# Kernel optimization log

Measured on AMD Instinct MI355X. Metric: run time of the kernel, lower is better.

The kernel has to match this reference:

```python
import jax, jax.numpy as jnp
import numpy as np

B, N, C, H, M, CC = 8, 1024, 1280, 20, 77, 768
FF = 4 * C
AQ_BITS = 8
W_BITS = 8


def fq_sym(x, bits=AQ_BITS):
    # per-tensor symmetric fake quant with straight-through estimator
    qmax = 2.0 ** (bits - 1) - 1.0
    delta = jnp.maximum(jnp.max(jnp.abs(x)), 1e-8) / qmax
    q = jnp.clip(jnp.round(x / delta), -qmax - 1.0, qmax) * delta
    return x + jax.lax.stop_gradient(q - x)


def fq_zero(x, bits=W_BITS):
    # asymmetric, always_zero (zero point = 0): for softmax probs in [0,1]
    levels = 2.0 ** bits - 1.0
    delta = jnp.maximum(jnp.max(x), 1e-8) / levels
    q = jnp.clip(jnp.round(x / delta), 0.0, levels) * delta
    return x + jax.lax.stop_gradient(q - x)


def layer_norm(x, g, b, eps=1e-5):
    mu = jnp.mean(x, axis=-1, keepdims=True)
    var = jnp.var(x, axis=-1, keepdims=True)
    return (x - mu) * jax.lax.rsqrt(var + eps) * g + b


def attention(x, ctx, Wq, Wk, Wv, Wo, bo, heads):
    b, n, c = x.shape
    m = ctx.shape[1]
    dh = c // heads
    q = fq_sym(x @ Wq)
    k = fq_sym(ctx @ Wk)
    v = fq_sym(ctx @ Wv)
    q = q.reshape(b, n, heads, dh).transpose(0, 2, 1, 3)
    k = k.reshape(b, m, heads, dh).transpose(0, 2, 1, 3)
    v = v.reshape(b, m, heads, dh).transpose(0, 2, 1, 3)
    scores = jnp.einsum('bhnd,bhmd->bhnm', q, k) * (dh ** -0.5)
    w = jax.nn.softmax(scores, axis=-1)
    w = fq_zero(w)  # quantized softmax weights (forces explicit prob materialization)
    out = jnp.einsum('bhnm,bhmd->bhnd', w, v)
    out = out.transpose(0, 2, 1, 3).reshape(b, n, c)
    return out @ Wo + bo


def geglu_ff(x, W1, b1, W2, b2):
    h = x @ W1 + b1
    a, g = jnp.split(h, 2, axis=-1)
    return (a * jax.nn.gelu(g)) @ W2 + b2


def setup_inputs() -> dict:
    key = jax.random.key(0)
    ks = jax.random.split(key, 16)
    s = 0.02
    return {
        'x': jax.random.normal(ks[0], (B, N, C), jnp.float32),
        'ctx': jax.random.normal(ks[1], (B, M, CC), jnp.float32),
        'ln1_g': jnp.ones((C,), jnp.float32), 'ln1_b': jnp.zeros((C,), jnp.float32),
        'ln2_g': jnp.ones((C,), jnp.float32), 'ln2_b': jnp.zeros((C,), jnp.float32),
        'ln3_g': jnp.ones((C,), jnp.float32), 'ln3_b': jnp.zeros((C,), jnp.float32),
        'Wq1': jax.random.normal(ks[2], (C, C), jnp.float32) * s,
        'Wk1': jax.random.normal(ks[3], (C, C), jnp.float32) * s,
        'Wv1': jax.random.normal(ks[4], (C, C), jnp.float32) * s,
        'Wo1': jax.random.normal(ks[5], (C, C), jnp.float32) * s,
        'bo1': jnp.zeros((C,), jnp.float32),
        'Wq2': jax.random.normal(ks[6], (C, C), jnp.float32) * s,
        'Wk2': jax.random.normal(ks[7], (CC, C), jnp.float32) * s,
        'Wv2': jax.random.normal(ks[8], (CC, C), jnp.float32) * s,
        'Wo2': jax.random.normal(ks[9], (C, C), jnp.float32) * s,
        'bo2': jnp.zeros((C,), jnp.float32),
        'Wff1': jax.random.normal(ks[10], (C, 2 * FF), jnp.float32) * s,
        'bff1': jnp.zeros((2 * FF,), jnp.float32),
        'Wff2': jax.random.normal(ks[11], (FF, C), jnp.float32) * s,
        'bff2': jnp.zeros((C,), jnp.float32),
        'heads': H,
    }


def reference(x, ctx, ln1_g, ln1_b, ln2_g, ln2_b, ln3_g, ln3_b,
              Wq1, Wk1, Wv1, Wo1, bo1, Wq2, Wk2, Wv2, Wo2, bo2,
              Wff1, bff1, Wff2, bff2, heads):
    h = attention(layer_norm(x, ln1_g, ln1_b), layer_norm(x, ln1_g, ln1_b),
                  Wq1, Wk1, Wv1, Wo1, bo1, heads)
    x = x + h
    h = attention(layer_norm(x, ln2_g, ln2_b), ctx, Wq2, Wk2, Wv2, Wo2, bo2, heads)
    x = x + h
    x = x + geglu_ff(layer_norm(x, ln3_g, ln3_b), Wff1, bff1, Wff2, bff2)
    return x
```

## Files before the change

kernel.cpp:

```cpp
#include <hip/hip_runtime.h>

typedef __attribute__((ext_vector_type(8))) short bf16x8;
typedef __attribute__((ext_vector_type(4))) float f32x4;

#define DEV __device__ __forceinline__
#define MF(A, B, CACC) CACC = __builtin_amdgcn_mfma_f32_16x16x32_bf16(A, B, CACC, 0, 0, 0)

DEV ushort f2b(float f) {
  unsigned u = __float_as_uint(f);
  u += 0x7fffu + ((u >> 16) & 1u);
  return (ushort)(u >> 16);
}
DEV float b2f(ushort u) { return __uint_as_float(((unsigned)u) << 16); }

DEV void gl_lds16(ushort* lds_base, const ushort* gp) {
  __builtin_amdgcn_global_load_lds(
      (__attribute__((address_space(1))) const void*)gp,
      (__attribute__((address_space(3))) void*)lds_base, 16, 0, 0);
}

__global__ void k_zero(unsigned* p, int n) {
  int i = blockIdx.x * blockDim.x + threadIdx.x;
  if (i < n) p[i] = 0u;
}

__global__ __launch_bounds__(256) void k_wt(const float* __restrict__ W,
                                            ushort* __restrict__ WT, int K, int N) {
  __shared__ float T[32][33];
  int k0 = blockIdx.y * 32, n0 = blockIdx.x * 32;
  int tx = threadIdx.x & 31, ty = threadIdx.x >> 5;
  #pragma unroll
  for (int r = ty; r < 32; r += 8) {
    int k = k0 + r, n = n0 + tx;
    T[r][tx] = (k < K && n < N) ? W[(size_t)k * N + n] : 0.f;
  }
  __syncthreads();
  #pragma unroll
  for (int r = ty; r < 32; r += 8) {
    int n = n0 + r, k = k0 + tx;
    if (n < N && k < K) WT[(size_t)n * K + k] = f2b(T[tx][r]);
  }
}

__global__ void k_cvt(const float* __restrict__ in, ushort* __restrict__ out, int n) {
  int i = blockIdx.x * 256 + threadIdx.x;
  if (i < n) out[i] = f2b(in[i]);
}

__global__ __launch_bounds__(256) void k_ln(const float* __restrict__ x,
    const float* __restrict__ g, const float* __restrict__ b,
    ushort* __restrict__ out) {
  const int C = 1280;
  int row = blockIdx.x, tid = threadIdx.x;
  const float* xr = x + (size_t)row * C;
  float v0 = xr[tid], v1 = xr[tid + 256], v2 = xr[tid + 512],
        v3 = xr[tid + 768], v4 = xr[tid + 1024];
  float s = v0 + v1 + v2 + v3 + v4;
  float ss = v0 * v0 + v1 * v1 + v2 * v2 + v3 * v3 + v4 * v4;
  #pragma unroll
  for (int off = 32; off; off >>= 1) {
    s += __shfl_down(s, off);
    ss += __shfl_down(ss, off);
  }
  __shared__ float red[8];
  __shared__ float mu_s, rstd_s;
  int wave = tid >> 6, lane = tid & 63;
  if (lane == 0) { red[wave] = s; red[4 + wave] = ss; }
  __syncthreads();
  if (tid == 0) {
    float S = red[0] + red[1] + red[2] + red[3];
    float SS = red[4] + red[5] + red[6] + red[7];
    float mu = S / C;
    float var = SS / C - mu * mu;
    mu_s = mu;
    rstd_s = rsqrtf(var + 1e-5f);
  }
  __syncthreads();
  float mu = mu_s, rstd = rstd_s;
  size_t o = (size_t)row * C + tid;
  out[o]        = f2b((v0 - mu) * rstd * g[tid]        + b[tid]);
  out[o + 256]  = f2b((v1 - mu) * rstd * g[tid + 256]  + b[tid + 256]);
  out[o + 512]  = f2b((v2 - mu) * rstd * g[tid + 512]  + b[tid + 512]);
  out[o + 768]  = f2b((v3 - mu) * rstd * g[tid + 768]  + b[tid + 768]);
  out[o + 1024] = f2b((v4 - mu) * rstd * g[tid + 1024] + b[tid + 1024]);
}

DEV void st1(float v, int r_, int c_, int ldc, const float* resid,
             float* Cf, ushort* Cb) {
  size_t o = (size_t)r_ * ldc + c_;
  if (resid) v += resid[o];
  if (Cf) Cf[o] = v;
  if (Cb) Cb[o] = f2b(v);
}
DEV float epi4(f32x4 v, int rbase, int c_, int M, int N, int ldc,
               const float* bias, const float* resid, float* Cf, ushort* Cb) {
  float v0 = v.x, v1 = v.y, v2 = v.z, v3 = v.w;
  float am = fmaxf(fmaxf(fabsf(v0), fabsf(v1)), fmaxf(fabsf(v2), fabsf(v3)));
  if (c_ < N) {
    float bb = bias ? bias[c_] : 0.f;
    v0 += bb; v1 += bb; v2 += bb; v3 += bb;
    if (rbase + 0 < M) st1(v0, rbase + 0, c_, ldc, resid, Cf, Cb);
    if (rbase + 1 < M) st1(v1, rbase + 1, c_, ldc, resid, Cf, Cb);
    if (rbase + 2 < M) st1(v2, rbase + 2, c_, ldc, resid, Cf, Cb);
    if (rbase + 3 < M) st1(v3, rbase + 3, c_, ldc, resid, Cf, Cb);
  }
  return am;
}

__global__ __launch_bounds__(256) void k_gemm(
    const ushort* __restrict__ A, int lda,
    const ushort* __restrict__ BT, int ldb,
    float* __restrict__ Cf, ushort* __restrict__ Cb, int ldc,
    const float* __restrict__ bias, const float* __restrict__ resid,
    unsigned* am_slot, int M, int N, int K, int slcN) {
  __shared__ __align__(16) ushort SAB[8192];
  int tid = threadIdx.x;
  int wave = tid >> 6, lane = tid & 63;
  int q = lane >> 4, mi = lane & 15;
  int wr = (wave >> 1) * 64, wc = (wave & 1) * 64;
  int bm0 = blockIdx.y * 128, bn0 = blockIdx.x * 128;
  f32x4 c00 = {}, c01 = {}, c02 = {}, c03 = {};
  f32x4 c10 = {}, c11 = {}, c12 = {}, c13 = {};
  f32x4 c20 = {}, c21 = {}, c22 = {}, c23 = {};
  f32x4 c30 = {}, c31 = {}, c32 = {}, c33 = {};
  for (int k0 = 0; k0 < K; k0 += 32) {
    __syncthreads();
    #pragma unroll
    for (int t = 0; t < 4; t++) {
      int c = wave * 256 + t * 64 + lane;
      const ushort* gp;
      if (c < 512) {
        int r = c >> 2, kc = (c & 3) << 3;
        int gr = bm0 + r; if (gr >= M) gr = M - 1;
        gp = A + (size_t)gr * lda + k0 + kc;
      } else {
        int c2 = c - 512;
        int r = c2 >> 2, kc = (c2 & 3) << 3;
        int gn = bn0 + r; if (gn >= N) gn = N - 1;
        gp = BT + (size_t)gn * ldb + k0 + kc;
      }
      gl_lds16(&SAB[(wave * 256 + t * 64) * 8], gp);
    }
    __syncthreads();
    const ushort* Ab = &SAB[(wr + mi) * 32 + q * 8];
    const ushort* Bb = &SAB[4096 + (wc + mi) * 32 + q * 8];
    bf16x8 a0 = *(const bf16x8*)(Ab);
    bf16x8 a1 = *(const bf16x8*)(Ab + 512);
    bf16x8 a2 = *(const bf16x8*)(Ab + 1024);
    bf16x8 a3 = *(const bf16x8*)(Ab + 1536);
    bf16x8 b0 = *(const bf16x8*)(Bb);
    bf16x8 b1 = *(const bf16x8*)(Bb + 512);
    bf16x8 b2 = *(const bf16x8*)(Bb + 1024);
    bf16x8 b3 = *(const bf16x8*)(Bb + 1536);
    MF(a0, b0, c00); MF(a0, b1, c01); MF(a0, b2, c02); MF(a0, b3, c03);
    MF(a1, b0, c10); MF(a1, b1, c11); MF(a1, b2, c12); MF(a1, b3, c13);
    MF(a2, b0, c20); MF(a2, b1, c21); MF(a2, b2, c22); MF(a2, b3, c23);
    MF(a3, b0, c30); MF(a3, b1, c31); MF(a3, b2, c32); MF(a3, b3, c33);
  }
  int rb = bm0 + wr + q * 4, cb = bn0 + wc + mi;
  float am = 0.f;
  am = fmaxf(am, epi4(c00, rb +  0, cb +  0, M, N, ldc, bias, resid, Cf, Cb));
  am = fmaxf(am, epi4(c01, rb +  0, cb + 16, M, N, ldc, bias, resid, Cf, Cb));
  am = fmaxf(am, epi4(c02, rb +  0, cb + 32, M, N, ldc, bias, resid, Cf, Cb));
  am = fmaxf(am, epi4(c03, rb +  0, cb + 48, M, N, ldc, bias, resid, Cf, Cb));
  am = fmaxf(am, epi4(c10, rb + 16, cb +  0, M, N, ldc, bias, resid, Cf, Cb));
  am = fmaxf(am, epi4(c11, rb + 16, cb + 16, M, N, ldc, bias, resid, Cf, Cb));
  am = fmaxf(am, epi4(c12, rb + 16, cb + 32, M, N, ldc, bias, resid, Cf, Cb));
  am = fmaxf(am, epi4(c13, rb + 16, cb + 48, M, N, ldc, bias, resid, Cf, Cb));
  am = fmaxf(am, epi4(c20, rb + 32, cb +  0, M, N, ldc, bias, resid, Cf, Cb));
  am = fmaxf(am, epi4(c21, rb + 32, cb + 16, M, N, ldc, bias, resid, Cf, Cb));
  am = fmaxf(am, epi4(c22, rb + 32, cb + 32, M, N, ldc, bias, resid, Cf, Cb));
  am = fmaxf(am, epi4(c23, rb + 32, cb + 48, M, N, ldc, bias, resid, Cf, Cb));
  am = fmaxf(am, epi4(c30, rb + 48, cb +  0, M, N, ldc, bias, resid, Cf, Cb));
  am = fmaxf(am, epi4(c31, rb + 48, cb + 16, M, N, ldc, bias, resid, Cf, Cb));
  am = fmaxf(am, epi4(c32, rb + 48, cb + 32, M, N, ldc, bias, resid, Cf, Cb));
  am = fmaxf(am, epi4(c33, rb + 48, cb + 48, M, N, ldc, bias, resid, Cf, Cb));
  if (am_slot) {
    #pragma unroll
    for (int off = 32; off; off >>= 1) am = fmaxf(am, __shfl_down(am, off));
    if (lane == 0) atomicMax(am_slot + bn0 / slcN, __float_as_uint(am));
  }
}

__global__ void k_quant8(const ushort* __restrict__ in, ushort* __restrict__ out,
                         const unsigned* __restrict__ slotb, int n8,
                         int colw8, int ld, int slcw) {
  int i = blockIdx.x * 256 + threadIdx.x;
  if (i >= n8) return;
  int row = i / colw8, c8 = i - row * colw8;
  int col = c8 * 8;
  size_t a = (size_t)row * ld + col;
  float delta = fmaxf(__uint_as_float(slotb[col / slcw]), 1e-8f) * (1.f / 127.f);
  bf16x8 v = *(const bf16x8*)(in + a);
  bf16x8 r;
  #pragma unroll
  for (int j = 0; j < 8; j++) {
    float x = b2f((ushort)v[j]);
    float y = fminf(fmaxf(rintf(x / delta), -128.f), 127.f) * delta;
    r[j] = (short)f2b(y);
  }
  *(bf16x8*)(out + a) = r;
}

__global__ __launch_bounds__(256) void k_vt(const ushort* __restrict__ vq,
    ushort* __restrict__ vT, int H, int Mr, int Mpad, int ldv) {
  __shared__ __align__(16) ushort T[64][72];
  int bh = blockIdx.y, b = bh / H, h = bh % H;
  int m0 = blockIdx.x * 64;
  int tid = threadIdx.x;
  #pragma unroll
  for (int c = tid; c < 512; c += 256) {
    int mm = c >> 3, dc = (c & 7) << 3;
    int m = m0 + mm;
    int4 val = make_int4(0, 0, 0, 0);
    if (m < Mr) val = *(const int4*)(vq + ((size_t)b * Mr + m) * ldv + h * 64 + dc);
    *(int4*)&T[mm][dc] = val;
  }
  __syncthreads();
  #pragma unroll
  for (int c = tid; c < 512; c += 256) {
    int dd = c >> 3, mc = (c & 7) << 3;
    unsigned w0 = (unsigned)T[mc + 0][dd] | ((unsigned)T[mc + 1][dd] << 16);
    unsigned w1 = (unsigned)T[mc + 2][dd] | ((unsigned)T[mc + 3][dd] << 16);
    unsigned w2 = (unsigned)T[mc + 4][dd] | ((unsigned)T[mc + 5][dd] << 16);
    unsigned w3 = (unsigned)T[mc + 6][dd] | ((unsigned)T[mc + 7][dd] << 16);
    int4 val = make_int4((int)w0, (int)w1, (int)w2, (int)w3);
    *(int4*)(vT + ((size_t)bh * 64 + dd) * Mpad + m0 + mc) = val;
  }
}

#define NEGI -3.0e38f
#define ONLUPD(SA, SB, SC, SD, MRUN, ZRUN) do { \
  float e0  = b0_  ? (SA).x * cs : NEGI; \
  float e1  = b1_  ? (SA).y * cs : NEGI; \
  float e2  = b2_  ? (SA).z * cs : NEGI; \
  float e3  = b3_  ? (SA).w * cs : NEGI; \
  float e4  = b4_  ? (SB).x * cs : NEGI; \
  float e5  = b5_  ? (SB).y * cs : NEGI; \
  float e6  = b6_  ? (SB).z * cs : NEGI; \
  float e7  = b7_  ? (SB).w * cs : NEGI; \
  float e8  = b8_  ? (SC).x * cs : NEGI; \
  float e9  = b9_  ? (SC).y * cs : NEGI; \
  float e10 = b10_ ? (SC).z * cs : NEGI; \
  float e11 = b11_ ? (SC).w * cs : NEGI; \
  float e12 = b12_ ? (SD).x * cs : NEGI; \
  float e13 = b13_ ? (SD).y * cs : NEGI; \
  float e14 = b14_ ? (SD).z * cs : NEGI; \
  float e15 = b15_ ? (SD).w * cs : NEGI; \
  float tm = fmaxf(fmaxf(fmaxf(fmaxf(e0, e1), fmaxf(e2, e3)), \
                         fmaxf(fmaxf(e4, e5), fmaxf(e6, e7))), \
                   fmaxf(fmaxf(fmaxf(e8, e9), fmaxf(e10, e11)), \
                         fmaxf(fmaxf(e12, e13), fmaxf(e14, e15)))); \
  float mn = fmaxf(MRUN, tm); \
  float zs = exp2f(e0 - mn)  + exp2f(e1 - mn)  + exp2f(e2 - mn)  + exp2f(e3 - mn) \
           + exp2f(e4 - mn)  + exp2f(e5 - mn)  + exp2f(e6 - mn)  + exp2f(e7 - mn) \
           + exp2f(e8 - mn)  + exp2f(e9 - mn)  + exp2f(e10 - mn) + exp2f(e11 - mn) \
           + exp2f(e12 - mn) + exp2f(e13 - mn) + exp2f(e14 - mn) + exp2f(e15 - mn); \
  ZRUN = ZRUN * exp2f(MRUN - mn) + zs; MRUN = mn; \
} while (0)

__global__ __launch_bounds__(256) void k_attn1(
    const ushort* __restrict__ qq, const ushort* __restrict__ kq,
    float2* __restrict__ rs, unsigned* __restrict__ pmax,
    int H, int N, int Mr, int ldq, int ldk, float cs) {
  __shared__ __align__(16) ushort Qs[128][72];
  __shared__ __align__(16) ushort Ks[64][72];
  int tid = threadIdx.x;
  int wave = tid >> 6, lane = tid & 63;
  int q = lane >> 4, mi = lane & 15;
  int bh = blockIdx.y, b = bh / H, h = bh % H;
  int r0 = blockIdx.x * 128;
  #pragma unroll
  for (int c = tid; c < 1024; c += 256) {
    int r = c >> 3, dc = (c & 7) << 3;
    *(int4*)&Qs[r][dc] = *(const int4*)(qq + ((size_t)b * N + r0 + r) * ldq + h * 64 + dc);
  }
  float m0r = NEGI, z0r = 0.f, m1r = NEGI, z1r = 0.f;
  int nt = (Mr + 63) >> 6;
  for (int mt = 0; mt < nt; mt++) {
    __syncthreads();
    #pragma unroll
    for (int c = tid; c < 512; c += 256) {
      int mm = c >> 3, dc = (c & 7) << 3;
      int m = mt * 64 + mm;
      int4 val = make_int4(0, 0, 0, 0);
      if (m < Mr) val = *(const int4*)(kq + ((size_t)b * Mr + m) * ldk + h * 64 + dc);
      *(int4*)&Ks[mm][dc] = val;
    }
    __syncthreads();
    f32x4 s0 = {}, s1 = {}, s2 = {}, s3 = {};
    f32x4 s4 = {}, s5 = {}, s6 = {}, s7 = {};
    #pragma unroll
    for (int kc = 0; kc < 2; kc++) {
      bf16x8 qv0 = *(const bf16x8*)&Qs[wave * 32 + mi][kc * 32 + q * 8];
      bf16x8 qv1 = *(const bf16x8*)&Qs[wave * 32 + 16 + mi][kc * 32 + q * 8];
      bf16x8 k0v = *(const bf16x8*)&Ks[mi][kc * 32 + q * 8];
      bf16x8 k1v = *(const bf16x8*)&Ks[16 + mi][kc * 32 + q * 8];
      bf16x8 k2v = *(const bf16x8*)&Ks[32 + mi][kc * 32 + q * 8];
      bf16x8 k3v = *(const bf16x8*)&Ks[48 + mi][kc * 32 + q * 8];
      MF(k0v, qv0, s0); MF(k1v, qv0, s1); MF(k2v, qv0, s2); MF(k3v, qv0, s3);
      MF(k0v, qv1, s4); MF(k1v, qv1, s5); MF(k2v, qv1, s6); MF(k3v, qv1, s7);
    }
    int kb = mt * 64 + q * 4;
    bool b0_  = kb + 0  < Mr, b1_  = kb + 1  < Mr, b2_  = kb + 2  < Mr, b3_  = kb + 3  < Mr;
    bool b4_  = kb + 16 < Mr, b5_  = kb + 17 < Mr, b6_  = kb + 18 < Mr, b7_  = kb + 19 < Mr;
    bool b8_  = kb + 32 < Mr, b9_  = kb + 33 < Mr, b10_ = kb + 34 < Mr, b11_ = kb + 35 < Mr;
    bool b12_ = kb + 48 < Mr, b13_ = kb + 49 < Mr, b14_ = kb + 50 < Mr, b15_ = kb + 51 < Mr;
    ONLUPD(s0, s1, s2, s3, m0r, z0r);
    ONLUPD(s4, s5, s6, s7, m1r, z1r);
  }
  float mo0 = fmaxf(m0r, __shfl_xor(m0r, 16));
  mo0 = fmaxf(mo0, __shfl_xor(mo0, 32));
  float zz0 = z0r * exp2f(m0r - mo0);
  zz0 += __shfl_xor(zz0, 16);
  zz0 += __shfl_xor(zz0, 32);
  float mo1 = fmaxf(m1r, __shfl_xor(m1r, 16));
  mo1 = fmaxf(mo1, __shfl_xor(mo1, 32));
  float zz1 = z1r * exp2f(m1r - mo1);
  zz1 += __shfl_xor(zz1, 16);
  zz1 += __shfl_xor(zz1, 32);
  if (q == 0) {
    float2 st; st.x = mo0; st.y = zz0;
    rs[(size_t)bh * N + r0 + wave * 32 + mi] = st;
    st.x = mo1; st.y = zz1;
    rs[(size_t)bh * N + r0 + wave * 32 + 16 + mi] = st;
  }
  float pm = fmaxf(1.f / zz0, 1.f / zz1);
  #pragma unroll
  for (int off = 32; off; off >>= 1) pm = fmaxf(pm, __shfl_down(pm, off));
  if (lane == 0) atomicMax(pmax, __float_as_uint(pm));
}

DEV ushort q8lvl(float s, float cs, float mc) {
  float p = fminf(rintf(exp2f(fmaf(s, cs, -mc))), 255.f);
  return (ushort)(__float_as_uint(p) >> 16);
}

#define PWR(RB, SA, SB, SC, SD, M0_, M1_, M2_, M3_) do { \
  Ps[(RB) + 0][mi]      = ok0 ? q8lvl((SA).x, cs, M0_) : (ushort)0; \
  Ps[(RB) + 1][mi]      = ok0 ? q8lvl((SA).y, cs, M1_) : (ushort)0; \
  Ps[(RB) + 2][mi]      = ok0 ? q8lvl((SA).z, cs, M2_) : (ushort)0; \
  Ps[(RB) + 3][mi]      = ok0 ? q8lvl((SA).w, cs, M3_) : (ushort)0; \
  Ps[(RB) + 0][16 + mi] = ok1 ? q8lvl((SB).x, cs, M0_) : (ushort)0; \
  Ps[(RB) + 1][16 + mi] = ok1 ? q8lvl((SB).y, cs, M1_) : (ushort)0; \
  Ps[(RB) + 2][16 + mi] = ok1 ? q8lvl((SB).z, cs, M2_) : (ushort)0; \
  Ps[(RB) + 3][16 + mi] = ok1 ? q8lvl((SB).w, cs, M3_) : (ushort)0; \
  Ps[(RB) + 0][32 + mi] = ok2 ? q8lvl((SC).x, cs, M0_) : (ushort)0; \
  Ps[(RB) + 1][32 + mi] = ok2 ? q8lvl((SC).y, cs, M1_) : (ushort)0; \
  Ps[(RB) + 2][32 + mi] = ok2 ? q8lvl((SC).z, cs, M2_) : (ushort)0; \
  Ps[(RB) + 3][32 + mi] = ok2 ? q8lvl((SC).w, cs, M3_) : (ushort)0; \
  Ps[(RB) + 0][48 + mi] = ok3 ? q8lvl((SD).x, cs, M0_) : (ushort)0; \
  Ps[(RB) + 1][48 + mi] = ok3 ? q8lvl((SD).y, cs, M1_) : (ushort)0; \
  Ps[(RB) + 2][48 + mi] = ok3 ? q8lvl((SD).z, cs, M2_) : (ushort)0; \
  Ps[(RB) + 3][48 + mi] = ok3 ? q8lvl((SD).w, cs, M3_) : (ushort)0; \
} while (0)

#define OSTORE(RRBASE, OA, OB, OC, OD) do { \
  size_t base = ((size_t)b * N + (RRBASE)) * C + h * 64 + mi; \
  ao[base]              = f2b((OA).x * delta); ao[base + C]          = f2b((OA).y * delta); \
  ao[base + 2 * C]      = f2b((OA).z * delta); ao[base + 3 * C]      = f2b((OA).w * delta); \
  ao[base + 16]         = f2b((OB).x * delta); ao[base + C + 16]     = f2b((OB).y * delta); \
  ao[base + 2 * C + 16] = f2b((OB).z * delta); ao[base + 3 * C + 16] = f2b((OB).w * delta); \
  ao[base + 32]         = f2b((OC).x * delta); ao[base + C + 32]     = f2b((OC).y * delta); \
  ao[base + 2 * C + 32] = f2b((OC).z * delta); ao[base + 3 * C + 32] = f2b((OC).w * delta); \
  ao[base + 48]         = f2b((OD).x * delta); ao[base + C + 48]     = f2b((OD).y * delta); \
  ao[base + 2 * C + 48] = f2b((OD).z * delta); ao[base + 3 * C + 48] = f2b((OD).w * delta); \
} while (0)

__global__ __launch_bounds__(256) void k_attn2(
    const ushort* __restrict__ qq, const ushort* __restrict__ kq,
    const ushort* __restrict__ vT, const float2* __restrict__ rs,
    const unsigned* __restrict__ pmax, ushort* __restrict__ ao,
    int H, int N, int Mr, int Mpad, int ldq, int ldk, float cs) {
  const int C = 1280;
  __shared__ __align__(16) ushort Qs[128][72];
  __shared__ __align__(16) ushort Ks[64][72];
  __shared__ __align__(16) ushort Vs[64][72];
  __shared__ __align__(16) ushort Ps[128][72];
  int tid = threadIdx.x;
  int wave = tid >> 6, lane = tid & 63;
  int q = lane >> 4, mi = lane & 15;
  int bh = blockIdx.y, b = bh / H, h = bh % H;
  int r0 = blockIdx.x * 128;
  #pragma unroll
  for (int c = tid; c < 1024; c += 256) {
    int r = c >> 3, dc = (c & 7) << 3;
    *(int4*)&Qs[r][dc] = *(const int4*)(qq + ((size_t)b * N + r0 + r) * ldq + h * 64 + dc);
  }
  int rb0 = wave * 32 + q * 4, rb1 = rb0 + 16;
  float delta = fmaxf(__uint_as_float(*pmax), 1e-8f) * (1.f / 255.f);
  float ldl = __log2f(delta);
  float2 u0 = rs[(size_t)bh * N + r0 + rb0 + 0];
  float2 u1 = rs[(size_t)bh * N + r0 + rb0 + 1];
  float2 u2 = rs[(size_t)bh * N + r0 + rb0 + 2];
  float2 u3 = rs[(size_t)bh * N + r0 + rb0 + 3];
  float2 u4 = rs[(size_t)bh * N + r0 + rb1 + 0];
  float2 u5 = rs[(size_t)bh * N + r0 + rb1 + 1];
  float2 u6 = rs[(size_t)bh * N + r0 + rb1 + 2];
  float2 u7 = rs[(size_t)bh * N + r0 + rb1 + 3];
  float mc0 = u0.x + __log2f(u0.y) + ldl;
  float mc1 = u1.x + __log2f(u1.y) + ldl;
  float mc2 = u2.x + __log2f(u2.y) + ldl;
  float mc3 = u3.x + __log2f(u3.y) + ldl;
  float mc4 = u4.x + __log2f(u4.y) + ldl;
  float mc5 = u5.x + __log2f(u5.y) + ldl;
  float mc6 = u6.x + __log2f(u6.y) + ldl;
  float mc7 = u7.x + __log2f(u7.y) + ldl;
  f32x4 o0 = {}, o1 = {}, o2 = {}, o3 = {};
  f32x4 o4 = {}, o5 = {}, o6 = {}, o7 = {};
  int nt = (Mr + 63) >> 6;
  for (int mt = 0; mt < nt; mt++) {
    __syncthreads();
    #pragma unroll
    for (int c = tid; c < 512; c += 256) {
      int mm = c >> 3, dc = (c & 7) << 3;
      int m = mt * 64 + mm;
      int4 val = make_int4(0, 0, 0, 0);
      if (m < Mr) val = *(const int4*)(kq + ((size_t)b * Mr + m) * ldk + h * 64 + dc);
      *(int4*)&Ks[mm][dc] = val;
      *(int4*)&Vs[mm][dc] = *(const int4*)(vT + ((size_t)bh * 64 + mm) * Mpad + mt * 64 + dc);
    }
    __syncthreads();
    f32x4 s0 = {}, s1 = {}, s2 = {}, s3 = {};
    f32x4 s4 = {}, s5 = {}, s6 = {}, s7 = {};
    #pragma unroll
    for (int kc = 0; kc < 2; kc++) {
      bf16x8 aq0 = *(const bf16x8*)&Qs[wave * 32 + mi][kc * 32 + q * 8];
      bf16x8 aq1 = *(const bf16x8*)&Qs[wave * 32 + 16 + mi][kc * 32 + q * 8];
      bf16x8 k0v = *(const bf16x8*)&Ks[mi][kc * 32 + q * 8];
      bf16x8 k1v = *(const bf16x8*)&Ks[16 + mi][kc * 32 + q * 8];
      bf16x8 k2v = *(const bf16x8*)&Ks[32 + mi][kc * 32 + q * 8];
      bf16x8 k3v = *(const bf16x8*)&Ks[48 + mi][kc * 32 + q * 8];
      MF(aq0, k0v, s0); MF(aq0, k1v, s1); MF(aq0, k2v, s2); MF(aq0, k3v, s3);
      MF(aq1, k0v, s4); MF(aq1, k1v, s5); MF(aq1, k2v, s6); MF(aq1, k3v, s7);
    }
    int mlim = Mr - mt * 64;
    bool ok0 = (mi      < mlim);
    bool ok1 = (16 + mi < mlim);
    bool ok2 = (32 + mi < mlim);
    bool ok3 = (48 + mi < mlim);
    PWR(rb0, s0, s1, s2, s3, mc0, mc1, mc2, mc3);
    PWR(rb1, s4, s5, s6, s7, mc4, mc5, mc6, mc7);
    asm volatile("s_waitcnt lgkmcnt(0)" ::: "memory");
    __builtin_amdgcn_sched_barrier(0);
    #pragma unroll
    for (int kc = 0; kc < 2; kc++) {
      bf16x8 ap0 = *(const bf16x8*)&Ps[wave * 32 + mi][kc * 32 + q * 8];
      bf16x8 ap1 = *(const bf16x8*)&Ps[wave * 32 + 16 + mi][kc * 32 + q * 8];
      bf16x8 v0 = *(const bf16x8*)&Vs[mi][kc * 32 + q * 8];
      bf16x8 v1 = *(const bf16x8*)&Vs[16 + mi][kc * 32 + q * 8];
      bf16x8 v2 = *(const bf16x8*)&Vs[32 + mi][kc * 32 + q * 8];
      bf16x8 v3 = *(const bf16x8*)&Vs[48 + mi][kc * 32 + q * 8];
      MF(ap0, v0, o0); MF(ap0, v1, o1); MF(ap0, v2, o2); MF(ap0, v3, o3);
      MF(ap1, v0, o4); MF(ap1, v1, o5); MF(ap1, v2, o6); MF(ap1, v3, o7);
    }
  }
  int rr0 = r0 + wave * 32 + q * 4;
  OSTORE(rr0, o0, o1, o2, o3);
  OSTORE(rr0 + 16, o4, o5, o6, o7);
}

#define BAR __builtin_amdgcn_s_barrier()
#define LGKM0 do { asm volatile("s_waitcnt lgkmcnt(0)" ::: "memory"); \
                   __builtin_amdgcn_sched_barrier(0); } while (0)
#define VM6 asm volatile("s_waitcnt vmcnt(6)" ::: "memory")
#define VM0 asm volatile("s_waitcnt vmcnt(0)" ::: "memory")
#define PRIO1 __builtin_amdgcn_s_setprio(1)
#define PRIO0 __builtin_amdgcn_s_setprio(0)

#define RDA01(P) do { \
  fa00 = *(const bf16x8*)&(P)[c0];        fa01 = *(const bf16x8*)&(P)[c1]; \
  fa10 = *(const bf16x8*)&(P)[1024 + c0]; fa11 = *(const bf16x8*)&(P)[1024 + c1]; } while (0)
#define RDA23(P) do { \
  fa20 = *(const bf16x8*)&(P)[2048 + c0]; fa21 = *(const bf16x8*)&(P)[2048 + c1]; \
  fa30 = *(const bf16x8*)&(P)[3072 + c0]; fa31 = *(const bf16x8*)&(P)[3072 + c1]; } while (0)
#define RDB(P, H) do { \
  b00 = *(const bf16x8*)&(P)[(H) + c0];        b01 = *(const bf16x8*)&(P)[(H) + c1]; \
  b10 = *(const bf16x8*)&(P)[(H) + 1024 + c0]; b11 = *(const bf16x8*)&(P)[(H) + 1024 + c1]; \
  b20 = *(const bf16x8*)&(P)[(H) + 2048 + c0]; b21 = *(const bf16x8*)&(P)[(H) + 2048 + c1]; \
  b30 = *(const bf16x8*)&(P)[(H) + 3072 + c0]; b31 = *(const bf16x8*)&(P)[(H) + 3072 + c1]; } while (0)
#define RDB8(P) RDB(P, 0)

#define MM8(AX0, AX1, AY0, AY1, C0, C1, C2, C3, D0, D1, D2, D3) \
  MF(AX0, b00, C0); MF(AX1, b01, C0); MF(AX0, b10, C1); MF(AX1, b11, C1); \
  MF(AX0, b20, C2); MF(AX1, b21, C2); MF(AX0, b30, C3); MF(AX1, b31, C3); \
  MF(AY0, b00, D0); MF(AY1, b01, D0); MF(AY0, b10, D1); MF(AY1, b11, D1); \
  MF(AY0, b20, D2); MF(AY1, b21, D2); MF(AY0, b30, D3); MF(AY1, b31, D3)

#define GB8(AP, BP, DB, KT) \
  RDA01(AP); RDB8(BP); \
  stB(DB, KT, 0); stB(DB, KT, 1); stA(DB, KT, 0); \
  BAR; LGKM0; \
  PRIO1; MM8(fa00, fa01, fa10, fa11, c00, c01, c02, c03, c10, c11, c12, c13); PRIO0; \
  BAR; \
  RDA23(AP); \
  stA(DB, KT, 1); stA(DB, KT, 2); stA(DB, KT, 3); \
  BAR; LGKM0; \
  PRIO1; MM8(fa20, fa21, fa30, fa31, c20, c21, c22, c23, c30, c31, c32, c33); PRIO0; \
  VM6; BAR;

#define GT8(AP, BP) \
  RDA01(AP); RDB8(BP); \
  BAR; LGKM0; \
  PRIO1; MM8(fa00, fa01, fa10, fa11, c00, c01, c02, c03, c10, c11, c12, c13); PRIO0; \
  BAR; \
  RDA23(AP); \
  BAR; LGKM0; \
  PRIO1; MM8(fa20, fa21, fa30, fa31, c20, c21, c22, c23, c30, c31, c32, c33); PRIO0;

__global__ __launch_bounds__(512) void k_gemm8(
    const ushort* __restrict__ A, int lda,
    const ushort* __restrict__ BT, int ldb,
    float* __restrict__ Cf, ushort* __restrict__ Cb, int ldc,
    const float* __restrict__ bias, const float* __restrict__ resid,
    unsigned* am_slot, int M, int N, int K, int slcN) {
  __shared__ __align__(16) ushort SAB[73728];
  int tid = threadIdx.x;
  int wave = tid >> 6, lane = tid & 63;
  int q = lane >> 4, mi = lane & 15;
  int wm = wave >> 1, wn = wave & 1;
  int lr = lane >> 3;
  int lc = ((lane & 7) ^ lr) * 8;

  int NBN = N >> 7;
  int nblk = (M >> 8) * NBN;
  int cpx = nblk >> 3;
  int wg = blockIdx.x;
  int swz = (wg & 7) * cpx + (wg >> 3);
  int bm0 = (swz / NBN) << 8, bn0 = (swz % NBN) << 7;

  const int swzr = (mi & 7) * 8;
  int c0 = (q * 8) ^ swzr, c1 = (32 + q * 8) ^ swzr;
  const ushort* A0p = &SAB[(wm * 64 + mi) * 64];
  const ushort* B0p = &SAB[16384 + (wn * 64 + mi) * 64];
  const ushort* A1p = A0p + 24576; const ushort* B1p = B0p + 24576;
  const ushort* A2p = A0p + 49152; const ushort* B2p = B0p + 49152;

  const ushort* gA = A  + (size_t)(bm0 + wave * 8 + lr) * lda + lc;
  const ushort* gB = BT + (size_t)(bn0 + wave * 8 + lr) * ldb + lc;
  ushort* lA = &SAB[wave * 512];
  ushort* lB = &SAB[16384 + wave * 512];

  auto stA = [&](int bb, int kt, int call) {
    gl_lds16(lA + bb * 24576 + call * 4096,
             gA + (size_t)call * 64 * lda + (size_t)kt * 64);
  };
  auto stB = [&](int bb, int kt, int call) {
    gl_lds16(lB + bb * 24576 + call * 4096,
             gB + (size_t)call * 64 * ldb + (size_t)kt * 64);
  };

  f32x4 c00 = {}, c01 = {}, c02 = {}, c03 = {};
  f32x4 c10 = {}, c11 = {}, c12 = {}, c13 = {};
  f32x4 c20 = {}, c21 = {}, c22 = {}, c23 = {};
  f32x4 c30 = {}, c31 = {}, c32 = {}, c33 = {};
  bf16x8 fa00, fa01, fa10, fa11, fa20, fa21, fa30, fa31;
  bf16x8 b00, b01, b10, b11, b20, b21, b30, b31;

  stB(0, 0, 0); stB(0, 0, 1);
  stA(0, 0, 0); stA(0, 0, 1); stA(0, 0, 2); stA(0, 0, 3);
  stB(1, 1, 0); stB(1, 1, 1);
  stA(1, 1, 0); stA(1, 1, 1); stA(1, 1, 2); stA(1, 1, 3);
  VM6; BAR;

  int NT = K >> 6, NTm = NT - 2;
  for (int t = 0; t < NTm; t += 3) {
    GB8(A0p, B0p, 2, t + 2);
    GB8(A1p, B1p, 0, t + 3);
    GB8(A2p, B2p, 1, t + 4);
  }
  GT8(A0p, B0p);
  VM0; BAR;
  GT8(A1p, B1p);

  int rb = bm0 + wm * 64 + q * 4, cb = bn0 + wn * 64 + mi;
  float am = 0.f;
  am = fmaxf(am, epi4(c00, rb +  0, cb +  0, M, N, ldc, bias, resid, Cf, Cb));
  am = fmaxf(am, epi4(c01, rb +  0, cb + 16, M, N, ldc, bias, resid, Cf, Cb));
  am = fmaxf(am, epi4(c02, rb +  0, cb + 32, M, N, ldc, bias, resid, Cf, Cb));
  am = fmaxf(am, epi4(c03, rb +  0, cb + 48, M, N, ldc, bias, resid, Cf, Cb));
  am = fmaxf(am, epi4(c10, rb + 16, cb +  0, M, N, ldc, bias, resid, Cf, Cb));
  am = fmaxf(am, epi4(c11, rb + 16, cb + 16, M, N, ldc, bias, resid, Cf, Cb));
  am = fmaxf(am, epi4(c12, rb + 16, cb + 32, M, N, ldc, bias, resid, Cf, Cb));
  am = fmaxf(am, epi4(c13, rb + 16, cb + 48, M, N, ldc, bias, resid, Cf, Cb));
  am = fmaxf(am, epi4(c20, rb + 32, cb +  0, M, N, ldc, bias, resid, Cf, Cb));
  am = fmaxf(am, epi4(c21, rb + 32, cb + 16, M, N, ldc, bias, resid, Cf, Cb));
  am = fmaxf(am, epi4(c22, rb + 32, cb + 32, M, N, ldc, bias, resid, Cf, Cb));
  am = fmaxf(am, epi4(c23, rb + 32, cb + 48, M, N, ldc, bias, resid, Cf, Cb));
  am = fmaxf(am, epi4(c30, rb + 48, cb +  0, M, N, ldc, bias, resid, Cf, Cb));
  am = fmaxf(am, epi4(c31, rb + 48, cb + 16, M, N, ldc, bias, resid, Cf, Cb));
  am = fmaxf(am, epi4(c32, rb + 48, cb + 32, M, N, ldc, bias, resid, Cf, Cb));
  am = fmaxf(am, epi4(c33, rb + 48, cb + 48, M, N, ldc, bias, resid, Cf, Cb));
  if (am_slot) {
    #pragma unroll
    for (int off = 32; off; off >>= 1) am = fmaxf(am, __shfl_down(am, off));
    if (lane == 0) atomicMax(am_slot + bn0 / slcN, __float_as_uint(am));
  }
}

DEV ushort ggel(float a, float g) {
  float u = 1.5957691216057308f * g * (1.f + 0.044715f * g * g);
  float s = 1.f / (1.f + __expf(-u));
  return f2b(a * g * s);
}
DEV void epi4g(f32x4 va, f32x4 vg, size_t base, float ba, float bg,
               ushort* __restrict__ GG) {
  GG[base]         = ggel(va.x + ba, vg.x + bg);
  GG[base + 5120]  = ggel(va.y + ba, vg.y + bg);
  GG[base + 10240] = ggel(va.z + ba, vg.z + bg);
  GG[base + 15360] = ggel(va.w + ba, vg.w + bg);
}
#define EPIN(nn, P0, Q0, P1, Q1, P2, Q2, P3, Q3) do { \
  int cg = colBase + nn * 16 + mi; \
  float ba = bias[cg], bg = bias[5120 + cg]; \
  size_t b0_ = (size_t)rowBase * 5120 + cg; \
  epi4g(P0, Q0, b0_,             ba, bg, GG); \
  epi4g(P1, Q1, b0_ + 16 * 5120, ba, bg, GG); \
  epi4g(P2, Q2, b0_ + 32 * 5120, ba, bg, GG); \
  epi4g(P3, Q3, b0_ + 48 * 5120, ba, bg, GG); \
} while (0)

__global__ __launch_bounds__(512) void k_ff1_8p(
    const ushort* __restrict__ A,
    const ushort* __restrict__ BT,
    const float* __restrict__ bias,
    ushort* __restrict__ GG) {
  __shared__ __align__(16) ushort SAB[65536];
  int tid = threadIdx.x;
  int wave = tid >> 6, lane = tid & 63;
  int q = lane >> 4, mi = lane & 15;
  int wm = wave >> 1, wn = wave & 1;
  int lr = lane >> 3;
  int lc = ((lane & 7) ^ lr) * 8;

  int wg = blockIdx.x;
  int swz = (wg & 7) * 160 + (wg >> 3);
  int bm0 = (swz & 31) * 256, bn0 = (swz >> 5) * 128;

  const int swzr = (mi & 7) * 8;
  int c0 = (q * 8) ^ swzr, c1 = (32 + q * 8) ^ swzr;
  const ushort* A0p = &SAB[(wm * 64 + mi) * 64];
  const ushort* B0p = &SAB[16384 + (wn * 64 + mi) * 64];
  const ushort* A1p = A0p + 32768;
  const ushort* B1p = B0p + 32768;

  const ushort* gA  = A  + (size_t)(bm0 + wave * 8 + lr) * 1280 + lc;
  const ushort* gBa = BT + (size_t)(bn0 + wave * 8 + lr) * 1280 + lc;
  const ushort* gBg = BT + (size_t)(5120 + bn0 + wave * 8 + lr) * 1280 + lc;
  ushort* lA = &SAB[wave * 512];
  ushort* lB = &SAB[16384 + wave * 512];

  auto stA = [&](int bb, int kt, int call) {
    gl_lds16(lA + bb * 32768 + call * 4096,
             gA + (size_t)call * 81920 + (size_t)kt * 64);
  };
  auto stBa = [&](int bb, int kt, int call) {
    gl_lds16(lB + bb * 32768 + call * 4096,
             gBa + (size_t)call * 81920 + (size_t)kt * 64);
  };
  auto stBg = [&](int bb, int kt, int call) {
    gl_lds16(lB + bb * 32768 + (call + 2) * 4096,
             gBg + (size_t)call * 81920 + (size_t)kt * 64);
  };

  f32x4 cA00 = {}, cA01 = {}, cA02 = {}, cA03 = {};
  f32x4 cA10 = {}, cA11 = {}, cA12 = {}, cA13 = {};
  f32x4 cA20 = {}, cA21 = {}, cA22 = {}, cA23 = {};
  f32x4 cA30 = {}, cA31 = {}, cA32 = {}, cA33 = {};
  f32x4 cG00 = {}, cG01 = {}, cG02 = {}, cG03 = {};
  f32x4 cG10 = {}, cG11 = {}, cG12 = {}, cG13 = {};
  f32x4 cG20 = {}, cG21 = {}, cG22 = {}, cG23 = {};
  f32x4 cG30 = {}, cG31 = {}, cG32 = {}, cG33 = {};
  bf16x8 fa00, fa01, fa10, fa11, fa20, fa21, fa30, fa31;
  bf16x8 b00, b01, b10, b11, b20, b21, b30, b31;

  stBa(0, 0, 0); stBa(0, 0, 1); stBg(0, 0, 0); stBg(0, 0, 1);
  stA(0, 0, 0); stA(0, 0, 1); stA(0, 0, 2); stA(0, 0, 3);
  stBa(1, 1, 0); stBa(1, 1, 1);
  stA(1, 1, 0); stA(1, 1, 1); stA(1, 1, 2); stA(1, 1, 3);
  VM6; BAR;

  for (int it = 0; it < 10; ++it) {
    int t1 = 2 * it + 1;
    int s0 = t1 + 1; if (s0 > 19) s0 = 19;
    int s1 = t1 + 2; if (s1 > 19) s1 = 19;
    RDA01(A0p); RDB(B0p, 0);
    stBg(1, t1, 0); stBg(1, t1, 1);
    BAR; LGKM0;
    PRIO1; MM8(fa00, fa01, fa10, fa11, cA00, cA01, cA02, cA03,
               cA10, cA11, cA12, cA13); PRIO0;
    BAR;
    RDA23(A0p);
    stBa(0, s0, 0); stBa(0, s0, 1);
    BAR; LGKM0;
    PRIO1; MM8(fa20, fa21, fa30, fa31, cA20, cA21, cA22, cA23,
               cA30, cA31, cA32, cA33); PRIO0;
    BAR;
    RDB(B0p, 8192);
    stA(0, s0, 0); stA(0, s0, 1);
    BAR; LGKM0;
    PRIO1; MM8(fa00, fa01, fa10, fa11, cG00, cG01, cG02, cG03,
               cG10, cG11, cG12, cG13); PRIO0;
    BAR;
    stA(0, s0, 2); stA(0, s0, 3);
    BAR;
    PRIO1; MM8(fa20, fa21, fa30, fa31, cG20, cG21, cG22, cG23,
               cG30, cG31, cG32, cG33); PRIO0;
    VM6; BAR;
    RDA01(A1p); RDB(B1p, 0);
    stBg(0, s0, 0); stBg(0, s0, 1);
    BAR; LGKM0;
    PRIO1; MM8(fa00, fa01, fa10, fa11, cA00, cA01, cA02, cA03,
               cA10, cA11, cA12, cA13); PRIO0;
    BAR;
    RDA23(A1p);
    stBa(1, s1, 0); stBa(1, s1, 1);
    BAR; LGKM0;
    PRIO1; MM8(fa20, fa21, fa30, fa31, cA20, cA21, cA22, cA23,
               cA30, cA31, cA32, cA33); PRIO0;
    BAR;
    RDB(B1p, 8192);
    stA(1, s1, 0); stA(1, s1, 1);
    BAR; LGKM0;
    PRIO1; MM8(fa00, fa01, fa10, fa11, cG00, cG01, cG02, cG03,
               cG10, cG11, cG12, cG13); PRIO0;
    BAR;
    stA(1, s1, 2); stA(1, s1, 3);
    BAR;
    PRIO1; MM8(fa20, fa21, fa30, fa31, cG20, cG21, cG22, cG23,
               cG30, cG31, cG32, cG33); PRIO0;
    VM6; BAR;
  }

  int colBase = bn0 + wn * 64;
  int rowBase = bm0 + wm * 64 + q * 4;
  EPIN(0, cA00, cG00, cA10, cG10, cA20, cG20, cA30, cG30);
  EPIN(1, cA01, cG01, cA11, cG11, cA21, cG21, cA31, cG31);
  EPIN(2, cA02, cG02, cA12, cG12, cA22, cG22, cA32, cG32);
  EPIN(3, cA03, cG03, cA13, cG13, cA23, cG23, cA33, cG33);
}

extern "C" void kernel_launch(void* const* d_in, const int* in_sizes, int n_in,
                              void* d_out, int out_size, void* d_ws, size_t ws_size,
                              hipStream_t stream) {
  const float* x_in = (const float*)d_in[0];
  const float* ctx  = (const float*)d_in[1];
  const float* ln1g = (const float*)d_in[2];
  const float* ln1b = (const float*)d_in[3];
  const float* ln2g = (const float*)d_in[4];
  const float* ln2b = (const float*)d_in[5];
  const float* ln3g = (const float*)d_in[6];
  const float* ln3b = (const float*)d_in[7];
  const float* Wq1  = (const float*)d_in[8];
  const float* Wk1  = (const float*)d_in[9];
  const float* Wv1  = (const float*)d_in[10];
  const float* Wo1  = (const float*)d_in[11];
  const float* bo1  = (const float*)d_in[12];
  const float* Wq2  = (const float*)d_in[13];
  const float* Wk2  = (const float*)d_in[14];
  const float* Wv2  = (const float*)d_in[15];
  const float* Wo2  = (const float*)d_in[16];
  const float* bo2  = (const float*)d_in[17];
  const float* Wff1 = (const float*)d_in[18];
  const float* bff1 = (const float*)d_in[19];
  const float* Wff2 = (const float*)d_in[20];
  const float* bff2 = (const float*)d_in[21];
  float* out = (float*)d_out;

  const int NR = 8192;
  const int C = 1280, H = 20, Nseq = 1024, CC = 768;
  const int MR2 = 616;
  const float CS = 0.18033688011112042f;

  char* ws = (char*)d_ws;
  size_t off = 0;
  auto alloc = [&](size_t bytes) -> void* {
    void* p = ws + off;
    off += (bytes + 255) & ~(size_t)255;
    return p;
  };
  unsigned* scal = (unsigned*)alloc(64);
  ushort* Wq1T  = (ushort*)alloc((size_t)C * C * 2);
  ushort* Wk1T  = (ushort*)alloc((size_t)C * C * 2);
  ushort* Wv1T  = (ushort*)alloc((size_t)C * C * 2);
  ushort* Wo1T  = (ushort*)alloc((size_t)C * C * 2);
  ushort* Wq2T  = (ushort*)alloc((size_t)C * C * 2);
  ushort* Wk2T  = (ushort*)alloc((size_t)C * CC * 2);
  ushort* Wv2T  = (ushort*)alloc((size_t)C * CC * 2);
  ushort* Wo2T  = (ushort*)alloc((size_t)C * C * 2);
  ushort* WF1T  = (ushort*)alloc((size_t)10240 * C * 2);
  ushort* WF2T  = (ushort*)alloc((size_t)C * 5120 * 2);
  ushort* LN    = (ushort*)alloc((size_t)NR * C * 2);
  size_t regionR = off;
  ushort* QKV   = (ushort*)alloc((size_t)NR * 3840 * 2);
  ushort* VT    = (ushort*)alloc((size_t)160 * 64 * 1024 * 2);
  float2* RS    = (float2*)alloc((size_t)160 * 1024 * 8);
  ushort* CTXB  = (ushort*)alloc((size_t)MR2 * CC * 2);
  ushort* KV2   = (ushort*)alloc((size_t)MR2 * 2560 * 2);
  size_t need = off;
  ushort* AO = LN;
  ushort* GG = (ushort*)(ws + regionR);
  if (ws_size < need) return;

  k_zero<<<1, 64, 0, stream>>>(scal, 8);
  k_wt<<<dim3(40, 40), 256, 0, stream>>>(Wq1, Wq1T, C, C);
  k_wt<<<dim3(40, 40), 256, 0, stream>>>(Wk1, Wk1T, C, C);
  k_wt<<<dim3(40, 40), 256, 0, stream>>>(Wv1, Wv1T, C, C);
  k_wt<<<dim3(40, 40), 256, 0, stream>>>(Wo1, Wo1T, C, C);
  k_wt<<<dim3(40, 40), 256, 0, stream>>>(Wq2, Wq2T, C, C);
  k_wt<<<dim3(40, 24), 256, 0, stream>>>(Wk2, Wk2T, CC, C);
  k_wt<<<dim3(40, 24), 256, 0, stream>>>(Wv2, Wv2T, CC, C);
  k_wt<<<dim3(40, 40), 256, 0, stream>>>(Wo2, Wo2T, C, C);
  k_wt<<<dim3(320, 40), 256, 0, stream>>>(Wff1, WF1T, C, 10240);
  k_wt<<<dim3(40, 160), 256, 0, stream>>>(Wff2, WF2T, 5120, C);

  k_ln<<<NR, 256, 0, stream>>>(x_in, ln1g, ln1b, LN);
  k_gemm8<<<dim3(960), 512, 0, stream>>>(LN, C, Wq1T, C, nullptr, QKV, 3840,
                                         nullptr, nullptr, scal + 0, NR, 3840, C, 1280);
  k_quant8<<<(NR * 3840 / 8 + 255) / 256, 256, 0, stream>>>(QKV, QKV, scal + 0,
                                                            NR * 480, 480, 3840, 1280);
  k_vt<<<dim3(16, 160), 256, 0, stream>>>(QKV + 2560, VT, H, 1024, 1024, 3840);
  k_attn1<<<dim3(8, 160), 256, 0, stream>>>(QKV, QKV + 1280, RS, scal + 3,
                                            H, Nseq, 1024, 3840, 3840, CS);
  k_attn2<<<dim3(8, 160), 256, 0, stream>>>(QKV, QKV + 1280, VT, RS, scal + 3, AO,
                                            H, Nseq, 1024, 1024, 3840, 3840, CS);
  k_gemm8<<<dim3(320), 512, 0, stream>>>(AO, C, Wo1T, C, out, nullptr, C,
                                         bo1, x_in, nullptr, NR, C, C, C);

  k_ln<<<NR, 256, 0, stream>>>(out, ln2g, ln2b, LN);
  k_gemm8<<<dim3(320), 512, 0, stream>>>(LN, C, Wq2T, C, nullptr, QKV, 3840,
                                         nullptr, nullptr, scal + 4, NR, C, C, C);
  k_quant8<<<(NR * C / 8 + 255) / 256, 256, 0, stream>>>(QKV, QKV, scal + 4,
                                                         NR * 160, 160, 3840, 1280);
  k_cvt<<<(MR2 * CC + 255) / 256, 256, 0, stream>>>(ctx, CTXB, MR2 * CC);
  k_gemm<<<dim3(20, 5), 256, 0, stream>>>(CTXB, CC, Wk2T, CC, nullptr, KV2, 2560,
                                          nullptr, nullptr, scal + 5, MR2, 2560, CC, 1280);
  k_quant8<<<(MR2 * 2560 / 8 + 255) / 256, 256, 0, stream>>>(KV2, KV2, scal + 5,
                                                             MR2 * 320, 320, 2560, 1280);
  k_vt<<<dim3(2, 160), 256, 0, stream>>>(KV2 + 1280, VT, H, 77, 128, 2560);
  k_attn1<<<dim3(8, 160), 256, 0, stream>>>(QKV, KV2, RS, scal + 7,
                                            H, Nseq, 77, 3840, 2560, CS);
  k_attn2<<<dim3(8, 160), 256, 0, stream>>>(QKV, KV2, VT, RS, scal + 7, AO,
                                            H, Nseq, 77, 128, 3840, 2560, CS);
  k_gemm8<<<dim3(320), 512, 0, stream>>>(AO, C, Wo2T, C, out, nullptr, C,
                                         bo2, out, nullptr, NR, C, C, C);

  k_ln<<<NR, 256, 0, stream>>>(out, ln3g, ln3b, LN);
  k_ff1_8p<<<dim3(1280), 512, 0, stream>>>(LN, WF1T, bff1, GG);
  k_gemm8<<<dim3(320), 512, 0, stream>>>(GG, 5120, WF2T, 5120, out, nullptr, C,
                                         bff2, out, nullptr, NR, C, 5120, C);
}
```

Measured before the change: 1.551 ms.

## Double-buffer K/V tiles in attention kernels via async global-to-LDS loads

```diff
diff --git a/kernel.cpp b/kernel.cpp
--- a/kernel.cpp
+++ b/kernel.cpp
@@ -230,6 +230,12 @@
 }
 
 #define NEGI -3.0e38f
+#define VMA4 asm volatile("s_waitcnt vmcnt(4)" ::: "memory")
+#define VMA2 asm volatile("s_waitcnt vmcnt(2)" ::: "memory")
+#define VMA0 asm volatile("s_waitcnt vmcnt(0)" ::: "memory")
+#define LGK0 asm volatile("s_waitcnt lgkmcnt(0)" ::: "memory")
+#define RBAR __builtin_amdgcn_s_barrier()
+
 #define ONLUPD(SA, SB, SC, SD, MRUN, ZRUN) do { \
   float e0  = b0_  ? (SA).x * cs : NEGI; \
   float e1  = b1_  ? (SA).y * cs : NEGI; \
@@ -264,7 +270,7 @@
     float2* __restrict__ rs, unsigned* __restrict__ pmax,
     int H, int N, int Mr, int ldq, int ldk, float cs) {
   __shared__ __align__(16) ushort Qs[128][72];
-  __shared__ __align__(16) ushort Ks[64][72];
+  __shared__ __align__(16) ushort KL[2][4096];
   int tid = threadIdx.x;
   int wave = tid >> 6, lane = tid & 63;
   int q = lane >> 4, mi = lane & 15;
@@ -275,29 +281,39 @@
     int r = c >> 3, dc = (c & 7) << 3;
     *(int4*)&Qs[r][dc] = *(const int4*)(qq + ((size_t)b * N + r0 + r) * ldq + h * 64 + dc);
   }
+  int lr8 = lane >> 3;
+  int ck = (lane & 7) ^ lr8;
+  const ushort* kbase = kq + (size_t)b * Mr * ldk + h * 64 + ck * 8;
+  auto stK = [&](int mt, int bb) {
+    #pragma unroll
+    for (int c = 0; c < 2; c++) {
+      int base8 = c * 4 + wave;
+      int m = mt * 64 + base8 * 8 + lr8; if (m >= Mr) m = Mr - 1;
+      gl_lds16(&KL[bb][base8 * 512], kbase + (size_t)m * ldk);
+    }
+  };
+  int nt = (Mr + 63) >> 6;
+  stK(0, 0);
+  if (nt > 1) { stK(1, 1); VMA2; } else VMA0;
+  LGK0;
+  RBAR;
+
   float m0r = NEGI, z0r = 0.f, m1r = NEGI, z1r = 0.f;
-  int nt = (Mr + 63) >> 6;
+  int co0 = (q ^ (mi & 7)) * 8;
+  int co1 = ((4 + q) ^ (mi & 7)) * 8;
   for (int mt = 0; mt < nt; mt++) {
-    __syncthreads();
-    #pragma unroll
-    for (int c = tid; c < 512; c += 256) {
-      int mm = c >> 3, dc = (c & 7) << 3;
-      int m = mt * 64 + mm;
-      int4 val = make_int4(0, 0, 0, 0);
-      if (m < Mr) val = *(const int4*)(kq + ((size_t)b * Mr + m) * ldk + h * 64 + dc);
-      *(int4*)&Ks[mm][dc] = val;
-    }
-    __syncthreads();
+    const ushort* KB = &KL[mt & 1][0];
     f32x4 s0 = {}, s1 = {}, s2 = {}, s3 = {};
     f32x4 s4 = {}, s5 = {}, s6 = {}, s7 = {};
     #pragma unroll
     for (int kc = 0; kc < 2; kc++) {
+      int co = kc ? co1 : co0;
       bf16x8 qv0 = *(const bf16x8*)&Qs[wave * 32 + mi][kc * 32 + q * 8];
       bf16x8 qv1 = *(const bf16x8*)&Qs[wave * 32 + 16 + mi][kc * 32 + q * 8];
-      bf16x8 k0v = *(const bf16x8*)&Ks[mi][kc * 32 + q * 8];
-      bf16x8 k1v = *(const bf16x8*)&Ks[16 + mi][kc * 32 + q * 8];
-      bf16x8 k2v = *(const bf16x8*)&Ks[32 + mi][kc * 32 + q * 8];
-      bf16x8 k3v = *(const bf16x8*)&Ks[48 + mi][kc * 32 + q * 8];
+      bf16x8 k0v = *(const bf16x8*)&KB[mi * 64 + co];
+      bf16x8 k1v = *(const bf16x8*)&KB[(16 + mi) * 64 + co];
+      bf16x8 k2v = *(const bf16x8*)&KB[(32 + mi) * 64 + co];
+      bf16x8 k3v = *(const bf16x8*)&KB[(48 + mi) * 64 + co];
       MF(k0v, qv0, s0); MF(k1v, qv0, s1); MF(k2v, qv0, s2); MF(k3v, qv0, s3);
       MF(k0v, qv1, s4); MF(k1v, qv1, s5); MF(k2v, qv1, s6); MF(k3v, qv1, s7);
     }
@@ -308,6 +324,10 @@
     bool b12_ = kb + 48 < Mr, b13_ = kb + 49 < Mr, b14_ = kb + 50 < Mr, b15_ = kb + 51 < Mr;
     ONLUPD(s0, s1, s2, s3, m0r, z0r);
     ONLUPD(s4, s5, s6, s7, m1r, z1r);
+    RBAR;
+    if (mt + 2 < nt) { stK(mt + 2, mt & 1); VMA2; }
+    else VMA0;
+    RBAR;
   }
   float mo0 = fmaxf(m0r, __shfl_xor(m0r, 16));
   mo0 = fmaxf(mo0, __shfl_xor(mo0, 32));
@@ -374,9 +394,9 @@
     int H, int N, int Mr, int Mpad, int ldq, int ldk, float cs) {
   const int C = 1280;
   __shared__ __align__(16) ushort Qs[128][72];
-  __shared__ __align__(16) ushort Ks[64][72];
-  __shared__ __align__(16) ushort Vs[64][72];
   __shared__ __align__(16) ushort Ps[128][72];
+  __shared__ __align__(16) ushort KL[2][4096];
+  __shared__ __align__(16) ushort VL[2][4096];
   int tid = threadIdx.x;
   int wave = tid >> 6, lane = tid & 63;
   int q = lane >> 4, mi = lane & 15;
@@ -387,6 +407,20 @@
     int r = c >> 3, dc = (c & 7) << 3;
     *(int4*)&Qs[r][dc] = *(const int4*)(qq + ((size_t)b * N + r0 + r) * ldq + h * 64 + dc);
   }
+  int lr8 = lane >> 3;
+  int ck = (lane & 7) ^ lr8;
+  const ushort* kbase = kq + (size_t)b * Mr * ldk + h * 64 + ck * 8;
+  const ushort* vbase = vT + ((size_t)bh * 64) * Mpad + ck * 8;
+  auto stKV = [&](int mt, int bb) {
+    #pragma unroll
+    for (int c = 0; c < 2; c++) {
+      int base8 = c * 4 + wave;
+      int rloc = base8 * 8 + lr8;
+      int m = mt * 64 + rloc; if (m >= Mr) m = Mr - 1;
+      gl_lds16(&KL[bb][base8 * 512], kbase + (size_t)m * ldk);
+      gl_lds16(&VL[bb][base8 * 512], vbase + (size_t)rloc * Mpad + mt * 64);
+    }
+  };
   int rb0 = wave * 32 + q * 4, rb1 = rb0 + 16;
   float delta = fmaxf(__uint_as_float(*pmax), 1e-8f) * (1.f / 255.f);
   float ldl = __log2f(delta);
@@ -406,31 +440,30 @@
   float mc5 = u5.x + __log2f(u5.y) + ldl;
   float mc6 = u6.x + __log2f(u6.y) + ldl;
   float mc7 = u7.x + __log2f(u7.y) + ldl;
+  int nt = (Mr + 63) >> 6;
+  stKV(0, 0);
+  if (nt > 1) { stKV(1, 1); VMA4; } else VMA0;
+  LGK0;
+  RBAR;
+
   f32x4 o0 = {}, o1 = {}, o2 = {}, o3 = {};
   f32x4 o4 = {}, o5 = {}, o6 = {}, o7 = {};
-  int nt = (Mr + 63) >> 6;
+  int co0 = (q ^ (mi & 7)) * 8;
+  int co1 = ((4 + q) ^ (mi & 7)) * 8;
   for (int mt = 0; mt < nt; mt++) {
-    __syncthreads();
-    #pragma unroll
-    for (int c = tid; c < 512; c += 256) {
-      int mm = c >> 3, dc = (c & 7) << 3;
-      int m = mt * 64 + mm;
-      int4 val = make_int4(0, 0, 0, 0);
-      if (m < Mr) val = *(const int4*)(kq + ((size_t)b * Mr + m) * ldk + h * 64 + dc);
-      *(int4*)&Ks[mm][dc] = val;
-      *(int4*)&Vs[mm][dc] = *(const int4*)(vT + ((size_t)bh * 64 + mm) * Mpad + mt * 64 + dc);
-    }
-    __syncthreads();
+    const ushort* KB = &KL[mt & 1][0];
+    const ushort* VB = &VL[mt & 1][0];
     f32x4 s0 = {}, s1 = {}, s2 = {}, s3 = {};
     f32x4 s4 = {}, s5 = {}, s6 = {}, s7 = {};
     #pragma unroll
     for (int kc = 0; kc < 2; kc++) {
+      int co = kc ? co1 : co0;
       bf16x8 aq0 = *(const bf16x8*)&Qs[wave * 32 + mi][kc * 32 + q * 8];
       bf16x8 aq1 = *(const bf16x8*)&Qs[wave * 32 + 16 + mi][kc * 32 + q * 8];
-      bf16x8 k0v = *(const bf16x8*)&Ks[mi][kc * 32 + q * 8];
-      bf16x8 k1v = *(const bf16x8*)&Ks[16 + mi][kc * 32 + q * 8];
-      bf16x8 k2v = *(const bf16x8*)&Ks[32 + mi][kc * 32 + q * 8];
-      bf16x8 k3v = *(const bf16x8*)&Ks[48 + mi][kc * 32 + q * 8];
+      bf16x8 k0v = *(const bf16x8*)&KB[mi * 64 + co];
+      bf16x8 k1v = *(const bf16x8*)&KB[(16 + mi) * 64 + co];
+      bf16x8 k2v = *(const bf16x8*)&KB[(32 + mi) * 64 + co];
+      bf16x8 k3v = *(const bf16x8*)&KB[(48 + mi) * 64 + co];
       MF(aq0, k0v, s0); MF(aq0, k1v, s1); MF(aq0, k2v, s2); MF(aq0, k3v, s3);
       MF(aq1, k0v, s4); MF(aq1, k1v, s5); MF(aq1, k2v, s6); MF(aq1, k3v, s7);
     }
@@ -441,19 +474,24 @@
     bool ok3 = (48 + mi < mlim);
     PWR(rb0, s0, s1, s2, s3, mc0, mc1, mc2, mc3);
     PWR(rb1, s4, s5, s6, s7, mc4, mc5, mc6, mc7);
-    asm volatile("s_waitcnt lgkmcnt(0)" ::: "memory");
+    LGK0;
     __builtin_amdgcn_sched_barrier(0);
     #pragma unroll
     for (int kc = 0; kc < 2; kc++) {
+      int co = kc ? co1 : co0;
       bf16x8 ap0 = *(const bf16x8*)&Ps[wave * 32 + mi][kc * 32 + q * 8];
       bf16x8 ap1 = *(const bf16x8*)&Ps[wave * 32 + 16 + mi][kc * 32 + q * 8];
-      bf16x8 v0 = *(const bf16x8*)&Vs[mi][kc * 32 + q * 8];
-      bf16x8 v1 = *(const bf16x8*)&Vs[16 + mi][kc * 32 + q * 8];
-      bf16x8 v2 = *(const bf16x8*)&Vs[32 + mi][kc * 32 + q * 8];
-      bf16x8 v3 = *(const bf16x8*)&Vs[48 + mi][kc * 32 + q * 8];
+      bf16x8 v0 = *(const bf16x8*)&VB[mi * 64 + co];
+      bf16x8 v1 = *(const bf16x8*)&VB[(16 + mi) * 64 + co];
+      bf16x8 v2 = *(const bf16x8*)&VB[(32 + mi) * 64 + co];
+      bf16x8 v3 = *(const bf16x8*)&VB[(48 + mi) * 64 + co];
       MF(ap0, v0, o0); MF(ap0, v1, o1); MF(ap0, v2, o2); MF(ap0, v3, o3);
       MF(ap1, v0, o4); MF(ap1, v1, o5); MF(ap1, v2, o6); MF(ap1, v3, o7);
     }
+    RBAR;
+    if (mt + 2 < nt) { stKV(mt + 2, mt & 1); VMA4; }
+    else VMA0;
+    RBAR;
   }
   int rr0 = r0 + wave * 32 + q * 4;
   OSTORE(rr0, o0, o1, o2, o3);
```

Result: no change. 1.544 ms (-0.5%).
